# Performance work log

Hardware: AMD Instinct MI355X
Metric: run time of the kernel (lower is better)

The kernel has to match this reference:

```python
import jax, jax.numpy as jnp
import numpy as np

N_NODES = 50000
N_EDGES = 600000
D_IN = 128
D_HID = 128
D_OUT = 64


def _graph_conv(x, src, dst, W, b, n):
    """DGL GraphConv, norm='both': out = D_in^{-1/2} A D_out^{-1/2} x W + b,
    degrees clamped to min 1. Weight applied before aggregation (equivalent,
    and what DGL does when in_feats >= out_feats)."""
    ones = jnp.ones(src.shape[0], x.dtype)
    deg_out = jnp.clip(jax.ops.segment_sum(ones, src, num_segments=n), 1.0)
    deg_in = jnp.clip(jax.ops.segment_sum(ones, dst, num_segments=n), 1.0)
    h = (x * jax.lax.rsqrt(deg_out)[:, None]) @ W          # [n, d_out]
    agg = jax.ops.segment_sum(h[src], dst, num_segments=n)  # SpMM: gather + scatter-add
    return agg * jax.lax.rsqrt(deg_in)[:, None] + b


def setup_inputs() -> dict:
    key = jax.random.key(0)
    ks = jax.random.split(key, 9)
    features = jax.random.normal(ks[0], (N_NODES, D_IN), jnp.float32)
    src1 = jax.random.randint(ks[1], (N_EDGES,), 0, N_NODES, jnp.int32)
    dst1 = jax.random.randint(ks[2], (N_EDGES,), 0, N_NODES, jnp.int32)
    src2 = jax.random.randint(ks[3], (N_EDGES,), 0, N_NODES, jnp.int32)
    dst2 = jax.random.randint(ks[4], (N_EDGES,), 0, N_NODES, jnp.int32)
    order_attn = jax.random.uniform(ks[5], (2,), jnp.float32)
    W1 = jax.random.normal(ks[6], (D_IN, D_HID), jnp.float32) * 0.05
    b1 = jnp.zeros((D_HID,), jnp.float32)
    W2 = jax.random.normal(ks[7], (D_HID, D_OUT), jnp.float32) * 0.05
    b2 = jnp.zeros((D_OUT,), jnp.float32)
    return {"features": features, "src1": src1, "dst1": dst1,
            "src2": src2, "dst2": dst2, "order_attn": order_attn,
            "W1": W1, "b1": b1, "W2": W2, "b2": b2}


def reference(features, src1, dst1, src2, dst2, order_attn, W1, b1, W2, b2):
    n = features.shape[0]
    # layer 1 on both graphs + weighted order-attention combine
    x11 = _graph_conv(features, src1, dst1, W1, b1, n)
    x12 = _graph_conv(features, src2, dst2, W1, b1, n)
    x1 = order_attn[0] * x11 + order_attn[1] * x12
    # layer 2 on both graphs + weighted combine
    x21 = _graph_conv(x1, src1, dst1, W2, b2, n)
    x22 = _graph_conv(x1, src2, dst2, W2, b2, n)
    return order_attn[0] * x21 + order_attn[1] * x22
```

## Files before the change

### kernel.cpp

```cpp
#include <hip/hip_runtime.h>

#define DINF 128
#define DHID 128
#define DOUTF 64

#define NSLICE 32
#define NSLICE_LOG 5
#define CHUNKC 12544
#define NCHUNKC 4
#define CHUNKF 3136
#define NCHUNKF 16

typedef unsigned short ushort_t;
typedef unsigned int uint_t;
typedef __attribute__((ext_vector_type(8))) short bf16x8;
typedef __attribute__((ext_vector_type(4))) float f32x4;

__device__ __forceinline__ ushort_t f2b(float x) {
    uint_t u = __float_as_uint(x);
    u += 0x7fffu + ((u >> 16) & 1u);
    return (ushort_t)(u >> 16);
}
__device__ __forceinline__ float b2f_lo(uint_t u) { return __uint_as_float(u << 16); }
__device__ __forceinline__ float b2f_hi(uint_t u) { return __uint_as_float(u & 0xffff0000u); }

__global__ void cnt_kernel(const int* __restrict__ s1, const int* __restrict__ d1,
                           const int* __restrict__ s2, const int* __restrict__ d2,
                           int* __restrict__ cntS, int* __restrict__ cntD, int N, int ne) {
    extern __shared__ int h[];
    int t = threadIdx.x;
    for (int j = t; j < CHUNKC; j += 1024) h[j] = 0;
    __syncthreads();

    int lo = blockIdx.x * CHUNKC;
    int q = blockIdx.y;
    bool isSrc = blockIdx.z == 0;
    int SL = (2 * ne) / NSLICE;
    int g = q >= (NSLICE / 2);
    const int* p = g ? (isSrc ? s2 : d2) : (isSrc ? s1 : d1);
    int base = g ? ne : 0;
    int e0 = q * SL - base;
    int e1 = e0 + SL;
    for (int i = e0 + t; i < e1; i += 1024) {
        int v = p[i] - lo;
        if ((unsigned)v < (unsigned)CHUNKC) atomicAdd(&h[v], 1);
    }
    __syncthreads();

    int* c = (isSrc ? cntS : cntD) + (size_t)q * N;
    for (int j = t; j < CHUNKC; j += 1024) {
        int node = lo + j;
        if (node < N) c[node] = h[j];
    }
}

__global__ void degred_kernel(const int* __restrict__ cntS, const int* __restrict__ cntD,
                              float* __restrict__ rs, int N) {
    int v = blockIdx.x * 256 + threadIdx.x;
    if (v >= N) return;
    int o1 = 0, i1 = 0, o2 = 0, i2 = 0;
    #pragma unroll
    for (int q = 0; q < NSLICE / 2; ++q) {
        o1 += cntS[(size_t)q * N + v];
        i1 += cntD[(size_t)q * N + v];
    }
    #pragma unroll
    for (int q = NSLICE / 2; q < NSLICE; ++q) {
        o2 += cntS[(size_t)q * N + v];
        i2 += cntD[(size_t)q * N + v];
    }
    rs[v]                  = rsqrtf(fmaxf((float)o1, 1.0f));
    rs[N + v]              = rsqrtf(fmaxf((float)i1, 1.0f));
    rs[2 * (size_t)N + v]  = rsqrtf(fmaxf((float)o2, 1.0f));
    rs[3 * (size_t)N + v]  = rsqrtf(fmaxf((float)i2, 1.0f));
}

__global__ void scan1_kernel(const int* __restrict__ cntD, int* __restrict__ offs,
                             int* __restrict__ bsum, int N, int m) {
    __shared__ int warp_sums[4];
    int t = threadIdx.x;
    int lane = t & 63;
    int wid = t >> 6;
    int base = blockIdx.x * 1024 + t * 4;

    int v4[4];
    int tot = 0;
    #pragma unroll
    for (int j = 0; j < 4; ++j) {
        int i = base + j;
        int d = 0;
        if (i < m) {
            int v = i >> NSLICE_LOG, q = i & (NSLICE - 1);
            d = cntD[(size_t)q * N + v];
        }
        v4[j] = d; tot += d;
    }
    int x = tot;
    #pragma unroll
    for (int off = 1; off < 64; off <<= 1) {
        int y = __shfl_up(x, off, 64);
        if (lane >= off) x += y;
    }
    if (lane == 63) warp_sums[wid] = x;
    __syncthreads();
    int wbase = 0;
    for (int w = 0; w < wid; ++w) wbase += warp_sums[w];
    int run = wbase + x - tot;
    #pragma unroll
    for (int j = 0; j < 4; ++j) {
        int i = base + j;
        if (i < m) offs[i] = run;
        run += v4[j];
    }
    if (t == 255) bsum[blockIdx.x] = run;
}

__global__ void scan2_kernel(int* __restrict__ bsum, int* __restrict__ offs, int nb, int m) {
    int lane = threadIdx.x;
    int run = 0;
    for (int base = 0; base < nb; base += 64) {
        int i = base + lane;
        int v = (i < nb) ? bsum[i] : 0;
        int x = v;
        #pragma unroll
        for (int off = 1; off < 64; off <<= 1) {
            int y = __shfl_up(x, off, 64);
            if (lane >= off) x += y;
        }
        if (i < nb) bsum[i] = run + x - v;
        run += __shfl(x, 63, 64);
    }
    if (lane == 0) offs[m] = run;
}

__global__ void scan3_kernel(int* __restrict__ offs, const int* __restrict__ bsum, int m) {
    int base = blockIdx.x * 1024 + threadIdx.x * 4;
    int add = bsum[blockIdx.x];
    #pragma unroll
    for (int j = 0; j < 4; ++j) {
        int i = base + j;
        if (i < m) offs[i] += add;
    }
}

__global__ void fill_kernel(const int* __restrict__ s1, const int* __restrict__ d1,
                            const int* __restrict__ s2, const int* __restrict__ d2,
                            const float* __restrict__ rs, const float* __restrict__ attn,
                            const int* __restrict__ offs, int2* __restrict__ csr,
                            int N, int ne) {
    extern __shared__ int cur[];
    int t = threadIdx.x;
    int lo = blockIdx.x * CHUNKF;
    int q = blockIdx.y;
    int lim = N - lo < CHUNKF ? N - lo : CHUNKF;
    for (int j = t; j < lim; j += 1024)
        cur[j] = offs[(size_t)(lo + j) * NSLICE + q];
    __syncthreads();

    int SL = (2 * ne) / NSLICE;
    int g = q >= (NSLICE / 2);
    const int* src = g ? s2 : s1;
    const int* dst = g ? d2 : d1;
    const float* rs_o = rs + (size_t)(2 * g) * N;
    const float* rs_i = rs + (size_t)(2 * g + 1) * N;
    float ag = attn[g];
    int base = g ? ne : 0;
    int e0 = q * SL - base;
    int e1 = e0 + SL;
    for (int i = e0 + t; i < e1; i += 1024) {
        int d = dst[i] - lo;
        if ((unsigned)d < (unsigned)lim) {
            int s = src[i];
            int pos = atomicAdd(&cur[d], 1);
            float w = ag * rs_i[lo + d] * rs_o[s];
            csr[pos] = make_int2(s, __float_as_int(w));
        }
    }
}

__global__ void wconv2_kernel(const float* __restrict__ W1, const float* __restrict__ W2,
                              ushort_t* __restrict__ Wt1, ushort_t* __restrict__ Wt2) {
    int tid = blockIdx.x * 256 + threadIdx.x;
    if (tid < 128 * 128) {
        int ncol = tid / 128, k = tid % 128;
        Wt1[tid] = f2b(W1[(size_t)k * 128 + ncol]);
    } else if (tid < 128 * 128 + 64 * 128) {
        int t2 = tid - 128 * 128;
        int ncol = t2 / 128, k = t2 % 128;
        Wt2[t2] = f2b(W2[(size_t)k * 64 + ncol]);
    }
}

template<int NOUT, bool F32IN>
__global__ __launch_bounds__(256) void mfma_gemm_kernel(const void* __restrict__ Xv,
                                                        const ushort_t* __restrict__ Wt,
                                                        ushort_t* __restrict__ Y, int n) {
    constexpr int CT = NOUT / 16;
    const int lane = threadIdx.x & 63;
    const int wv = threadIdx.x >> 6;
    const int row0 = blockIdx.x * 64 + wv * 16;
    const int arow = row0 + (lane & 15);
    const int arc = arow < n ? arow : (n - 1);

    f32x4 acc[CT];
    #pragma unroll
    for (int ct = 0; ct < CT; ++ct) acc[ct] = (f32x4)(0.f);

    #pragma unroll
    for (int kk = 0; kk < 4; ++kk) {
        const int k0 = kk * 32 + (lane >> 4) * 8;
        bf16x8 a;
        if (F32IN) {
            const float* xp = (const float*)Xv + (size_t)arc * 128 + k0;
            float4 u0 = *(const float4*)xp;
            float4 u1 = *(const float4*)(xp + 4);
            a[0] = (short)f2b(u0.x); a[1] = (short)f2b(u0.y);
            a[2] = (short)f2b(u0.z); a[3] = (short)f2b(u0.w);
            a[4] = (short)f2b(u1.x); a[5] = (short)f2b(u1.y);
            a[6] = (short)f2b(u1.z); a[7] = (short)f2b(u1.w);
        } else {
            a = *(const bf16x8*)((const ushort_t*)Xv + (size_t)arc * 128 + k0);
        }
        #pragma unroll
        for (int ct = 0; ct < CT; ++ct) {
            bf16x8 b = *(const bf16x8*)(Wt + (size_t)(ct * 16 + (lane & 15)) * 128 + k0);
            acc[ct] = __builtin_amdgcn_mfma_f32_16x16x32_bf16(a, b, acc[ct], 0, 0, 0);
        }
    }

    const int orow0 = row0 + (lane >> 4) * 4;
    const int col = lane & 15;
    #pragma unroll
    for (int ct = 0; ct < CT; ++ct) {
        #pragma unroll
        for (int r = 0; r < 4; ++r) {
            int row = orow0 + r;
            if (row < n) Y[(size_t)row * NOUT + ct * 16 + col] = f2b(acc[ct][r]);
        }
    }
}

__global__ void agg128_kernel(const ushort_t* __restrict__ V, const int* __restrict__ offs,
                              const int2* __restrict__ csr, const float* __restrict__ bias,
                              const float* __restrict__ attn, uint_t* __restrict__ out, int n) {
    int wid = (int)(((size_t)blockIdx.x * blockDim.x + threadIdx.x) >> 6);
    int lane = threadIdx.x & 63;
    if (wid >= n) return;
    int e0 = offs[(size_t)wid << NSLICE_LOG];
    int e1 = offs[((size_t)wid << NSLICE_LOG) + NSLICE];

    float acc0 = 0.f, acc1 = 0.f;
    int e = e0;
    for (; e + 8 <= e1; e += 8) {
        int2 cv[8]; uint_t u[8];
        #pragma unroll
        for (int j = 0; j < 8; ++j) cv[j] = csr[e + j];
        #pragma unroll
        for (int j = 0; j < 8; ++j)
            u[j] = ((const uint_t*)(V + (size_t)cv[j].x * 128))[lane];
        #pragma unroll
        for (int j = 0; j < 8; ++j) {
            float w = __int_as_float(cv[j].y);
            acc0 += w * b2f_lo(u[j]); acc1 += w * b2f_hi(u[j]);
        }
    }
    if (e + 4 <= e1) {
        int2 cv[4]; uint_t u[4];
        #pragma unroll
        for (int j = 0; j < 4; ++j) cv[j] = csr[e + j];
        #pragma unroll
        for (int j = 0; j < 4; ++j)
            u[j] = ((const uint_t*)(V + (size_t)cv[j].x * 128))[lane];
        #pragma unroll
        for (int j = 0; j < 4; ++j) {
            float w = __int_as_float(cv[j].y);
            acc0 += w * b2f_lo(u[j]); acc1 += w * b2f_hi(u[j]);
        }
        e += 4;
    }
    for (; e < e1; ++e) {
        int2 cv = csr[e];
        float w = __int_as_float(cv.y);
        uint_t u = ((const uint_t*)(V + (size_t)cv.x * 128))[lane];
        acc0 += w * b2f_lo(u); acc1 += w * b2f_hi(u);
    }

    float bs = attn[0] + attn[1];
    float2 bb = ((const float2*)bias)[lane];
    float o0 = acc0 + bs * bb.x;
    float o1 = acc1 + bs * bb.y;
    out[(size_t)wid * 64 + lane] = (uint_t)f2b(o0) | ((uint_t)f2b(o1) << 16);
}

__global__ void agg64_kernel(const ushort_t* __restrict__ V, const int* __restrict__ offs,
                             const int2* __restrict__ csr, const float* __restrict__ bias,
                             const float* __restrict__ attn, float* __restrict__ out, int n) {
    int wid = (int)(((size_t)blockIdx.x * blockDim.x + threadIdx.x) >> 6);
    int lane = threadIdx.x & 63;
    int half = lane >> 5;
    int hl = lane & 31;
    if (wid >= n) return;
    int e0 = offs[(size_t)wid << NSLICE_LOG];
    int e1 = offs[((size_t)wid << NSLICE_LOG) + NSLICE];

    float acc0 = 0.f, acc1 = 0.f;
    int e = e0;
    for (; e + 8 <= e1; e += 8) {
        int2 cv[4]; uint_t u[4];
        #pragma unroll
        for (int j = 0; j < 4; ++j) cv[j] = csr[e + 2 * j + half];
        #pragma unroll
        for (int j = 0; j < 4; ++j)
            u[j] = ((const uint_t*)(V + (size_t)cv[j].x * 64))[hl];
        #pragma unroll
        for (int j = 0; j < 4; ++j) {
            float w = __int_as_float(cv[j].y);
            acc0 += w * b2f_lo(u[j]); acc1 += w * b2f_hi(u[j]);
        }
    }
    for (; e + 2 <= e1; e += 2) {
        int2 cv = csr[e + half];
        float w = __int_as_float(cv.y);
        uint_t u = ((const uint_t*)(V + (size_t)cv.x * 64))[hl];
        acc0 += w * b2f_lo(u); acc1 += w * b2f_hi(u);
    }
    if (e < e1 && half == 0) {
        int2 cv = csr[e];
        float w = __int_as_float(cv.y);
        uint_t u = ((const uint_t*)(V + (size_t)cv.x * 64))[hl];
        acc0 += w * b2f_lo(u); acc1 += w * b2f_hi(u);
    }

    acc0 += __shfl_xor(acc0, 32, 64);
    acc1 += __shfl_xor(acc1, 32, 64);

    if (half == 0) {
        float bs = attn[0] + attn[1];
        float2 bb = ((const float2*)bias)[hl];
        float2 o = make_float2(acc0 + bs * bb.x, acc1 + bs * bb.y);
        ((float2*)(out + (size_t)wid * 64))[hl] = o;
    }
}

extern "C" void kernel_launch(void* const* d_in, const int* in_sizes, int n_in,
                              void* d_out, int out_size, void* d_ws, size_t ws_size,
                              hipStream_t stream) {
    const float* feat = (const float*)d_in[0];
    const int* src1   = (const int*)d_in[1];
    const int* dst1   = (const int*)d_in[2];
    const int* src2   = (const int*)d_in[3];
    const int* dst2   = (const int*)d_in[4];
    const float* attn = (const float*)d_in[5];
    const float* W1   = (const float*)d_in[6];
    const float* b1   = (const float*)d_in[7];
    const float* W2   = (const float*)d_in[8];
    const float* b2   = (const float*)d_in[9];
    float* out = (float*)d_out;

    const int N  = in_sizes[0] / DINF;
    const int NE = in_sizes[1];
    const int M  = NSLICE * N;
    const int NB2 = (M + 1023) / 1024;

    ushort_t* Wt1 = (ushort_t*)d_ws;
    ushort_t* Wt2 = Wt1 + 128 * 128;
    ushort_t* A   = Wt2 + 64 * 128;
    ushort_t* B   = A + (size_t)N * DHID;
    ushort_t* C   = B + (size_t)N * DHID;
    int* offs   = (int*)(C + (size_t)N * DOUTF);
    int* cntS   = offs + (M + 1);
    int* cntD   = cntS + M;
    float* rs   = (float*)(cntD + M);
    int* bsum   = (int*)(rs + 4 * (size_t)N);
    int2* csr   = (int2*)cntS;

    wconv2_kernel<<<(128 * 128 + 64 * 128 + 255) / 256, 256, 0, stream>>>(W1, W2, Wt1, Wt2);

    cnt_kernel<<<dim3(NCHUNKC, NSLICE, 2), 1024, CHUNKC * sizeof(int), stream>>>(
        src1, dst1, src2, dst2, cntS, cntD, N, NE);

    degred_kernel<<<(N + 255) / 256, 256, 0, stream>>>(cntS, cntD, rs, N);

    scan1_kernel<<<NB2, 256, 0, stream>>>(cntD, offs, bsum, N, M);
    scan2_kernel<<<1, 64, 0, stream>>>(bsum, offs, NB2, M);
    scan3_kernel<<<NB2, 256, 0, stream>>>(offs, bsum, M);

    fill_kernel<<<dim3(NCHUNKF, NSLICE), 1024, CHUNKF * sizeof(int), stream>>>(
        src1, dst1, src2, dst2, rs, attn, offs, csr, N, NE);

    int gb = (N + 63) / 64;
    int ab = (N + 3) / 4;
    mfma_gemm_kernel<DHID, true><<<gb, 256, 0, stream>>>(feat, Wt1, A, N);
    agg128_kernel<<<ab, 256, 0, stream>>>(A, offs, csr, b1, attn, (uint_t*)B, N);

    mfma_gemm_kernel<DOUTF, false><<<gb, 256, 0, stream>>>(B, Wt2, C, N);
    agg64_kernel<<<ab, 256, 0, stream>>>(C, offs, csr, b2, attn, out, N);
}
```

Before: 212.5 us.

## Store only source indices in CSR and compute edge weights during aggregation

The CSR fill now writes a 4-byte source index instead of an 8-byte (index, weight) pair, and reads dst with int4 vector loads. The aggregation kernels split each node's edge range at the graph boundary (slice 16), gather the per-source rsqrt degree on the fly, and apply the destination normalization and attention weight once per graph at the end. This halves CSR write and read traffic and removes per-edge weight arithmetic in fill. In exchange it adds an extra random 4-byte gather of rs per edge in both aggregation passes.

Measured after the change: 205.2 us. 3.4% less time.

```diff
diff --git a/kernel.cpp b/kernel.cpp
--- a/kernel.cpp
+++ b/kernel.cpp
@@ -145,8 +145,7 @@
 
 __global__ void fill_kernel(const int* __restrict__ s1, const int* __restrict__ d1,
                             const int* __restrict__ s2, const int* __restrict__ d2,
-                            const float* __restrict__ rs, const float* __restrict__ attn,
-                            const int* __restrict__ offs, int2* __restrict__ csr,
+                            const int* __restrict__ offs, int* __restrict__ csr,
                             int N, int ne) {
     extern __shared__ int cur[];
     int t = threadIdx.x;
@@ -161,19 +160,27 @@
     int g = q >= (NSLICE / 2);
     const int* src = g ? s2 : s1;
     const int* dst = g ? d2 : d1;
-    const float* rs_o = rs + (size_t)(2 * g) * N;
-    const float* rs_i = rs + (size_t)(2 * g + 1) * N;
-    float ag = attn[g];
     int base = g ? ne : 0;
     int e0 = q * SL - base;
+    int sl4 = SL & ~4095;
     int e1 = e0 + SL;
-    for (int i = e0 + t; i < e1; i += 1024) {
-        int d = dst[i] - lo;
-        if ((unsigned)d < (unsigned)lim) {
-            int s = src[i];
-            int pos = atomicAdd(&cur[d], 1);
-            float w = ag * rs_i[lo + d] * rs_o[s];
-            csr[pos] = make_int2(s, __float_as_int(w));
+
+    for (int i = e0 + t * 4; i < e0 + sl4; i += 4096) {
+        int4 d4 = *(const int4*)(dst + i);
+        #pragma unroll
+        for (int j = 0; j < 4; ++j) {
+            int dd = ((const int*)&d4)[j] - lo;
+            if ((unsigned)dd < (unsigned)lim) {
+                int pos = atomicAdd(&cur[dd], 1);
+                csr[pos] = src[i + j];
+            }
+        }
+    }
+    for (int i = e0 + sl4 + t; i < e1; i += 1024) {
+        int dd = dst[i] - lo;
+        if ((unsigned)dd < (unsigned)lim) {
+            int pos = atomicAdd(&cur[dd], 1);
+            csr[pos] = src[i];
         }
     }
 }
@@ -240,104 +247,133 @@
     }
 }
 
+__device__ __forceinline__ void consume128(const int* __restrict__ csr,
+                                           const float* __restrict__ rso,
+                                           const ushort_t* __restrict__ V, int lane,
+                                           int e0, int e1, float& acc0, float& acc1) {
+    int e = e0;
+    for (; e + 8 <= e1; e += 8) {
+        int sv[8]; float wv[8]; uint_t uv[8];
+        #pragma unroll
+        for (int j = 0; j < 8; ++j) sv[j] = csr[e + j];
+        #pragma unroll
+        for (int j = 0; j < 8; ++j) wv[j] = rso[sv[j]];
+        #pragma unroll
+        for (int j = 0; j < 8; ++j)
+            uv[j] = ((const uint_t*)(V + (size_t)sv[j] * 128))[lane];
+        #pragma unroll
+        for (int j = 0; j < 8; ++j) {
+            acc0 += wv[j] * b2f_lo(uv[j]); acc1 += wv[j] * b2f_hi(uv[j]);
+        }
+    }
+    if (e + 4 <= e1) {
+        int sv[4]; float wv[4]; uint_t uv[4];
+        #pragma unroll
+        for (int j = 0; j < 4; ++j) sv[j] = csr[e + j];
+        #pragma unroll
+        for (int j = 0; j < 4; ++j) wv[j] = rso[sv[j]];
+        #pragma unroll
+        for (int j = 0; j < 4; ++j)
+            uv[j] = ((const uint_t*)(V + (size_t)sv[j] * 128))[lane];
+        #pragma unroll
+        for (int j = 0; j < 4; ++j) {
+            acc0 += wv[j] * b2f_lo(uv[j]); acc1 += wv[j] * b2f_hi(uv[j]);
+        }
+        e += 4;
+    }
+    for (; e < e1; ++e) {
+        int s = csr[e];
+        float w = rso[s];
+        uint_t u = ((const uint_t*)(V + (size_t)s * 128))[lane];
+        acc0 += w * b2f_lo(u); acc1 += w * b2f_hi(u);
+    }
+}
+
 __global__ void agg128_kernel(const ushort_t* __restrict__ V, const int* __restrict__ offs,
-                              const int2* __restrict__ csr, const float* __restrict__ bias,
-                              const float* __restrict__ attn, uint_t* __restrict__ out, int n) {
+                              const int* __restrict__ csr, const float* __restrict__ rs,
+                              const float* __restrict__ bias, const float* __restrict__ attn,
+                              uint_t* __restrict__ out, int n) {
     int wid = (int)(((size_t)blockIdx.x * blockDim.x + threadIdx.x) >> 6);
     int lane = threadIdx.x & 63;
     if (wid >= n) return;
     int e0 = offs[(size_t)wid << NSLICE_LOG];
+    int eb = offs[((size_t)wid << NSLICE_LOG) + 16];
     int e1 = offs[((size_t)wid << NSLICE_LOG) + NSLICE];
 
-    float acc0 = 0.f, acc1 = 0.f;
+    float s10 = 0.f, s11 = 0.f, s20 = 0.f, s21 = 0.f;
+    consume128(csr, rs, V, lane, e0, eb, s10, s11);
+    consume128(csr, rs + 2 * (size_t)n, V, lane, eb, e1, s20, s21);
+
+    float f1 = attn[0] * rs[(size_t)n + wid];
+    float f2 = attn[1] * rs[3 * (size_t)n + wid];
+    float bs = attn[0] + attn[1];
+    float2 bb = ((const float2*)bias)[lane];
+    float o0 = f1 * s10 + f2 * s20 + bs * bb.x;
+    float o1 = f1 * s11 + f2 * s21 + bs * bb.y;
+    out[(size_t)wid * 64 + lane] = (uint_t)f2b(o0) | ((uint_t)f2b(o1) << 16);
+}
+
+__device__ __forceinline__ void consume64(const int* __restrict__ csr,
+                                          const float* __restrict__ rso,
+                                          const ushort_t* __restrict__ V, int hl, int half,
+                                          int e0, int e1, float& acc0, float& acc1) {
     int e = e0;
     for (; e + 8 <= e1; e += 8) {
-        int2 cv[8]; uint_t u[8];
-        #pragma unroll
-        for (int j = 0; j < 8; ++j) cv[j] = csr[e + j];
-        #pragma unroll
-        for (int j = 0; j < 8; ++j)
-            u[j] = ((const uint_t*)(V + (size_t)cv[j].x * 128))[lane];
-        #pragma unroll
-        for (int j = 0; j < 8; ++j) {
-            float w = __int_as_float(cv[j].y);
-            acc0 += w * b2f_lo(u[j]); acc1 += w * b2f_hi(u[j]);
-        }
-    }
-    if (e + 4 <= e1) {
-        int2 cv[4]; uint_t u[4];
-        #pragma unroll
-        for (int j = 0; j < 4; ++j) cv[j] = csr[e + j];
+        int sv[4]; float wv[4]; uint_t uv[4];
+        #pragma unroll
+        for (int j = 0; j < 4; ++j) sv[j] = csr[e + 2 * j + half];
+        #pragma unroll
+        for (int j = 0; j < 4; ++j) wv[j] = rso[sv[j]];
         #pragma unroll
         for (int j = 0; j < 4; ++j)
-            u[j] = ((const uint_t*)(V + (size_t)cv[j].x * 128))[lane];
+            uv[j] = ((const uint_t*)(V + (size_t)sv[j] * 64))[hl];
         #pragma unroll
         for (int j = 0; j < 4; ++j) {
-            float w = __int_as_float(cv[j].y);
-            acc0 += w * b2f_lo(u[j]); acc1 += w * b2f_hi(u[j]);
-        }
-        e += 4;
-    }
-    for (; e < e1; ++e) {
-        int2 cv = csr[e];
-        float w = __int_as_float(cv.y);
-        uint_t u = ((const uint_t*)(V + (size_t)cv.x * 128))[lane];
+            acc0 += wv[j] * b2f_lo(uv[j]); acc1 += wv[j] * b2f_hi(uv[j]);
+        }
+    }
+    for (; e + 2 <= e1; e += 2) {
+        int s = csr[e + half];
+        float w = rso[s];
+        uint_t u = ((const uint_t*)(V + (size_t)s * 64))[hl];
         acc0 += w * b2f_lo(u); acc1 += w * b2f_hi(u);
     }
-
-    float bs = attn[0] + attn[1];
-    float2 bb = ((const float2*)bias)[lane];
-    float o0 = acc0 + bs * bb.x;
-    float o1 = acc1 + bs * bb.y;
-    out[(size_t)wid * 64 + lane] = (uint_t)f2b(o0) | ((uint_t)f2b(o1) << 16);
+    if (e < e1 && half == 0) {
+        int s = csr[e];
+        float w = rso[s];
+        uint_t u = ((const uint_t*)(V + (size_t)s * 64))[hl];
+        acc0 += w * b2f_lo(u); acc1 += w * b2f_hi(u);
+    }
 }
 
 __global__ void agg64_kernel(const ushort_t* __restrict__ V, const int* __restrict__ offs,
-                             const int2* __restrict__ csr, const float* __restrict__ bias,
-                             const float* __restrict__ attn, float* __restrict__ out, int n) {
+                             const int* __restrict__ csr, const float* __restrict__ rs,
+                             const float* __restrict__ bias, const float* __restrict__ attn,
+                             float* __restrict__ out, int n) {
     int wid = (int)(((size_t)blockIdx.x * blockDim.x + threadIdx.x) >> 6);
     int lane = threadIdx.x & 63;
     int half = lane >> 5;
     int hl = lane & 31;
     if (wid >= n) return;
     int e0 = offs[(size_t)wid << NSLICE_LOG];
+    int eb = offs[((size_t)wid << NSLICE_LOG) + 16];
     int e1 = offs[((size_t)wid << NSLICE_LOG) + NSLICE];
 
-    float acc0 = 0.f, acc1 = 0.f;
-    int e = e0;
-    for (; e + 8 <= e1; e += 8) {
-        int2 cv[4]; uint_t u[4];
-        #pragma unroll
-        for (int j = 0; j < 4; ++j) cv[j] = csr[e + 2 * j + half];
-        #pragma unroll
-        for (int j = 0; j < 4; ++j)
-            u[j] = ((const uint_t*)(V + (size_t)cv[j].x * 64))[hl];
-        #pragma unroll
-        for (int j = 0; j < 4; ++j) {
-            float w = __int_as_float(cv[j].y);
-            acc0 += w * b2f_lo(u[j]); acc1 += w * b2f_hi(u[j]);
-        }
-    }
-    for (; e + 2 <= e1; e += 2) {
-        int2 cv = csr[e + half];
-        float w = __int_as_float(cv.y);
-        uint_t u = ((const uint_t*)(V + (size_t)cv.x * 64))[hl];
-        acc0 += w * b2f_lo(u); acc1 += w * b2f_hi(u);
-    }
-    if (e < e1 && half == 0) {
-        int2 cv = csr[e];
-        float w = __int_as_float(cv.y);
-        uint_t u = ((const uint_t*)(V + (size_t)cv.x * 64))[hl];
-        acc0 += w * b2f_lo(u); acc1 += w * b2f_hi(u);
-    }
-
-    acc0 += __shfl_xor(acc0, 32, 64);
-    acc1 += __shfl_xor(acc1, 32, 64);
+    float s10 = 0.f, s11 = 0.f, s20 = 0.f, s21 = 0.f;
+    consume64(csr, rs, V, hl, half, e0, eb, s10, s11);
+    consume64(csr, rs + 2 * (size_t)n, V, hl, half, eb, e1, s20, s21);
+
+    float f1 = attn[0] * rs[(size_t)n + wid];
+    float f2 = attn[1] * rs[3 * (size_t)n + wid];
+    float c0 = f1 * s10 + f2 * s20;
+    float c1 = f1 * s11 + f2 * s21;
+    c0 += __shfl_xor(c0, 32, 64);
+    c1 += __shfl_xor(c1, 32, 64);
 
     if (half == 0) {
         float bs = attn[0] + attn[1];
         float2 bb = ((const float2*)bias)[hl];
-        float2 o = make_float2(acc0 + bs * bb.x, acc1 + bs * bb.y);
+        float2 o = make_float2(c0 + bs * bb.x, c1 + bs * bb.y);
         ((float2*)(out + (size_t)wid * 64))[hl] = o;
     }
 }
@@ -372,7 +408,7 @@
     int* cntD   = cntS + M;
     float* rs   = (float*)(cntD + M);
     int* bsum   = (int*)(rs + 4 * (size_t)N);
-    int2* csr   = (int2*)cntS;
+    int* csr    = cntS;
 
     wconv2_kernel<<<(128 * 128 + 64 * 128 + 255) / 256, 256, 0, stream>>>(W1, W2, Wt1, Wt2);
 
@@ -386,13 +422,13 @@
     scan3_kernel<<<NB2, 256, 0, stream>>>(offs, bsum, M);
 
     fill_kernel<<<dim3(NCHUNKF, NSLICE), 1024, CHUNKF * sizeof(int), stream>>>(
-        src1, dst1, src2, dst2, rs, attn, offs, csr, N, NE);
+        src1, dst1, src2, dst2, offs, csr, N, NE);
 
     int gb = (N + 63) / 64;
     int ab = (N + 3) / 4;
     mfma_gemm_kernel<DHID, true><<<gb, 256, 0, stream>>>(feat, Wt1, A, N);
-    agg128_kernel<<<ab, 256, 0, stream>>>(A, offs, csr, b1, attn, (uint_t*)B, N);
+    agg128_kernel<<<ab, 256, 0, stream>>>(A, offs, csr, rs, b1, attn, (uint_t*)B, N);
 
     mfma_gemm_kernel<DOUTF, false><<<gb, 256, 0, stream>>>(B, Wt2, C, N);
-    agg64_kernel<<<ab, 256, 0, stream>>>(C, offs, csr, b2, attn, out, N);
-}
+    agg64_kernel<<<ab, 256, 0, stream>>>(C, offs, csr, rs, b2, attn, out, N);
+}
```
